# Performance work log

Measured on AMD Instinct MI355X. Metric: run time of the kernel, lower is better.

The kernel has to match this reference:

```python
import jax, jax.numpy as jnp
import numpy as np

N, P, G = 524288, 16, 8


def setup_inputs() -> dict:
    key = jax.random.key(0)
    k1, k2, k3, k4, k5 = jax.random.split(key, 5)
    # Strictly positive data (Box-Cox transform uses log / fractional powers)
    X = jax.random.uniform(k1, (N, P), dtype=jnp.float32) + 0.1
    # Box-Cox powers away from 0 to avoid division blow-up
    lambdas = jax.random.uniform(k2, (P, 1), dtype=jnp.float32) + 0.5
    # Means near the transformed-data range so densities don't underflow
    mus = 0.1 * jax.random.normal(k3, (G, P), dtype=jnp.float32) - 0.3
    # SPD covariances: 0.25*I + A A^T
    A = 0.05 * jax.random.normal(k4, (G, P, P), dtype=jnp.float32)
    sigmas = 0.25 * jnp.eye(P, dtype=jnp.float32)[None] + jnp.einsum('gpq,grq->gpr', A, A)
    w = jax.random.uniform(k5, (G, 1), dtype=jnp.float32)
    return {"X": X, "lambdas": lambdas, "mus": mus, "sigmas": sigmas, "w": w}


def reference(X, lambdas, mus, sigmas, w):
    # objective_fn of the GMM: negative log-likelihood of a Box-Cox GMM.
    n, p = X.shape
    lam = lambdas[:, 0]                                  # (p,)
    Xt = (X ** lam - 1.0) / lam                          # Box-Cox transform, (n,p)
    Sinv = jnp.linalg.inv(sigmas)                        # (G,p,p), once per component
    logdet = jnp.linalg.slogdet(sigmas)[1]               # (G,)
    d = Xt[:, None, :] - mus[None, :, :]                 # (n,G,p)
    quad = jnp.einsum('ngp,gpq,ngq->ng', d, Sinv, d)     # batched Mahalanobis, (n,G)
    lead = -0.5 * p * jnp.log(jnp.float32(2.0) * jnp.pi)
    jac = jnp.log(X) @ (lam - 1.0)                       # log-Jacobian of Box-Cox, (n,)
    ldens = -0.5 * quad + lead - 0.5 * logdet[None, :] + jac[:, None]  # (n,G)
    W = jax.nn.softmax(w[:, 0])                          # mixing proportions, (G,)
    mixed = (jnp.exp(ldens) * W).sum(-1)                 # (n,)
    return -jnp.log(mixed).sum()
```

## Files before the change

### kernel.cpp

```cpp
#include <hip/hip_runtime.h>
#include <hip/hip_bf16.h>


#define P 16
#define G 8

typedef short bf16x8 __attribute__((ext_vector_type(8)));
typedef unsigned u32x4v __attribute__((ext_vector_type(4)));
typedef float f32x16 __attribute__((ext_vector_type(16)));

__device__ __forceinline__ unsigned short f2bf(float f) {
    unsigned u = __builtin_bit_cast(unsigned, f);
    return (unsigned short)((u + 0x7FFFu + ((u >> 16) & 1u)) >> 16);
}

#define UFRAG_F 1024
#define WS_LC   1280
#define WS_LAM  1288
#define WS_LM1  1304
#define WS_RL   1320
#define WS_PART 4096

__global__ __launch_bounds__(128) void gmm_prep(const float* __restrict__ lambdas,
                                                const float* __restrict__ mus,
                                                const float* __restrict__ sigmas,
                                                const float* __restrict__ w,
                                                float* __restrict__ ws) {
    __shared__ float Ssh[G][P][P];
    __shared__ float Lsh[G][P][P];
    __shared__ float Vsh[G][P][P];
    __shared__ float u_sh[G][P];
    __shared__ float ldet[G];
    const int tid = threadIdx.x;
    const int g = tid >> 4;
    const int r = tid & 15;

    {
        const float4* src = (const float4*)(sigmas + g * P * P + r * P);
        float4* dst = (float4*)&Ssh[g][r][0];
        dst[0] = src[0]; dst[1] = src[1]; dst[2] = src[2]; dst[3] = src[3];
    }
    __syncthreads();

#pragma unroll
    for (int j = 0; j < P; ++j) {
        float s = Ssh[g][r][j];
#pragma unroll
        for (int k = 0; k < j; ++k) s -= Lsh[g][r][k] * Lsh[g][j][k];
        if (r == j) Lsh[g][j][j] = sqrtf(s);
        __syncthreads();
        if (r > j) Lsh[g][r][j] = s / Lsh[g][j][j];
        __syncthreads();
    }

    if (r == 0) {
        float ld = 0.f;
#pragma unroll
        for (int j = 0; j < P; ++j) ld += __logf(Lsh[g][j][j]);
        ldet[g] = 2.0f * ld;
    }

#pragma unroll
    for (int i = 0; i < P; ++i) {
        float s = 0.f;
#pragma unroll
        for (int k = 0; k < i; ++k) s += Lsh[g][i][k] * Vsh[g][k][r];
        const float rii = 1.0f / Lsh[g][i][i];
        Vsh[g][i][r] = (i == r) ? rii : ((i < r) ? 0.f : -s * rii);
    }
    __syncthreads();

    {
        float u = 0.f;
#pragma unroll
        for (int j = 0; j < P; ++j) u = fmaf(Vsh[g][r][j], mus[g * P + j], u);
        u_sh[g][r] = u;
    }
    __syncthreads();

    unsigned short* ws16 = (unsigned short*)ws;
    unsigned* wsu32 = (unsigned*)(ws + UFRAG_F);
#pragma unroll
    for (int pid = tid; pid < 256; pid += 128) {
        const int p = pid >> 6, ln = pid & 63;
        const int m = ln & 31, half = ln >> 5;
        const int grp = 2 * (pid >> 6) + (m >> 4), i = m & 15;
        unsigned short* dst = ws16 + (p * 64 + ln) * 8;
#pragma unroll
        for (int j = 0; j < 8; ++j) dst[j] = f2bf(Vsh[grp][i][half * 8 + j]);
        wsu32[p * 64 + ln] = (half == 0) ? (unsigned)f2bf(-u_sh[grp][i]) : 0u;
    }

    if (tid == 0) {
        float wm = w[0];
#pragma unroll
        for (int k = 1; k < G; ++k) wm = fmaxf(wm, w[k]);
        float s = 0.f;
#pragma unroll
        for (int k = 0; k < G; ++k) s += __expf(w[k] - wm);
        const float lse = wm + __logf(s);
        const float lead = -14.7030165f;
#pragma unroll
        for (int k = 0; k < G; ++k)
            ws[WS_LC + k] = (w[k] - lse) + lead - 0.5f * ldet[k];
    }
    if (tid < P) {
        float lam = lambdas[tid];
        ws[WS_LAM + tid] = lam;
        ws[WS_LM1 + tid] = lam - 1.0f;
        ws[WS_RL  + tid] = 1.0f / lam;
    }
}

__global__ __launch_bounds__(256, 4) void gmm_main(const float* __restrict__ X,
                                                   const float* __restrict__ ws,
                                                   float* __restrict__ partials,
                                                   int nrows) {
    __shared__ u32x4v sxt4[512];
    __shared__ float red[4];

    const int tid  = threadIdx.x;
    const int lane = tid & 63;
    const int wid  = tid >> 6;
    const unsigned short* ws16 = (const unsigned short*)ws;
    const unsigned* wsu32 = (const unsigned*)(ws + UFRAG_F);

    const bf16x8 av0 = *(const bf16x8*)(ws16 + (0 * 64 + lane) * 8);
    const bf16x8 av1 = *(const bf16x8*)(ws16 + (1 * 64 + lane) * 8);
    const bf16x8 av2 = *(const bf16x8*)(ws16 + (2 * 64 + lane) * 8);
    const bf16x8 av3 = *(const bf16x8*)(ws16 + (3 * 64 + lane) * 8);
    bf16x8 au0 = {0,0,0,0,0,0,0,0}; au0[0] = (short)wsu32[0 * 64 + lane];
    bf16x8 au1 = {0,0,0,0,0,0,0,0}; au1[0] = (short)wsu32[1 * 64 + lane];
    bf16x8 au2 = {0,0,0,0,0,0,0,0}; au2[0] = (short)wsu32[2 * 64 + lane];
    bf16x8 au3 = {0,0,0,0,0,0,0,0}; au3[0] = (short)wsu32[3 * 64 + lane];

    const int row = blockIdx.x * 256 + tid;
    const int rc = row < nrows ? row : nrows - 1;
    const float4* Xv = (const float4*)(X + (size_t)rc * P);
    const float4 A0 = Xv[0], A1 = Xv[1], A2 = Xv[2], A3 = Xv[3];

    float jac = 0.f;
#define XTP(i, xv_) \
    const float ln##i = __logf(xv_); \
    const float xt##i = (__expf(ws[WS_LAM + i] * ln##i) - 1.0f) * ws[WS_RL + i]; \
    jac = fmaf(ln##i, ws[WS_LM1 + i], jac);
    XTP(0, A0.x)  XTP(1, A0.y)  XTP(2, A0.z)  XTP(3, A0.w)
    XTP(4, A1.x)  XTP(5, A1.y)  XTP(6, A1.z)  XTP(7, A1.w)
    XTP(8, A2.x)  XTP(9, A2.y)  XTP(10, A2.z) XTP(11, A2.w)
    XTP(12, A3.x) XTP(13, A3.y) XTP(14, A3.z) XTP(15, A3.w)
#undef XTP

#define PK(h_, a_, b_) const unsigned w##h_ = (unsigned)f2bf(xt##a_) | ((unsigned)f2bf(xt##b_) << 16);
    PK(0, 0, 1)  PK(1, 2, 3)   PK(2, 4, 5)   PK(3, 6, 7)
    PK(4, 8, 9)  PK(5, 10, 11) PK(6, 12, 13) PK(7, 14, 15)
#undef PK
    {
        const u32x4v lo = {w0, w1, w2, w3};
        const u32x4v hi = {w4, w5, w6, w7};
        const int F = tid >> 5, c = tid & 31;
        sxt4[F * 64 + c]      = lo;
        sxt4[F * 64 + 32 + c] = hi;
    }
    __syncthreads();

    bf16x8 b1 = {0,0,0,0,0,0,0,0};
    if (lane < 32) b1[0] = (short)0x3F80;
    const bool h = (lane >= 32);

    float nll = 0.f;

#define PAIR(AV, AU, SA, SB) { \
    f32x16 acc = {}; \
    acc = __builtin_amdgcn_mfma_f32_32x32x16_bf16(AU, b1, acc, 0, 0, 0); \
    acc = __builtin_amdgcn_mfma_f32_32x32x16_bf16(AV, bx, acc, 0, 0, 0); \
    float sa = acc[0] * acc[0];    float sb = acc[8] * acc[8]; \
    sa = fmaf(acc[1], acc[1], sa); sb = fmaf(acc[9],  acc[9],  sb); \
    sa = fmaf(acc[2], acc[2], sa); sb = fmaf(acc[10], acc[10], sb); \
    sa = fmaf(acc[3], acc[3], sa); sb = fmaf(acc[11], acc[11], sb); \
    sa = fmaf(acc[4], acc[4], sa); sb = fmaf(acc[12], acc[12], sb); \
    sa = fmaf(acc[5], acc[5], sa); sb = fmaf(acc[13], acc[13], sb); \
    sa = fmaf(acc[6], acc[6], sa); sb = fmaf(acc[14], acc[14], sb); \
    sa = fmaf(acc[7], acc[7], sa); sb = fmaf(acc[15], acc[15], sb); \
    SA = sa; SB = sb; }

#define TILE(t_) { \
    const bf16x8 bx = __builtin_bit_cast(bf16x8, sxt4[(wid * 2 + t_) * 64 + lane]); \
    const float jn = __shfl(jac, t_ * 32 + (lane & 31), 64); \
    float pa0, pa1, pa2, pa3, pb0, pb1, pb2, pb3; \
    PAIR(av0, au0, pa0, pb0) PAIR(av1, au1, pa1, pb1) \
    PAIR(av2, au2, pa2, pb2) PAIR(av3, au3, pa3, pb3) \
    const float k0 = h ? pa2 : pa0, s0 = h ? pa0 : pa2; \
    const float k1 = h ? pb2 : pb0, s1 = h ? pb0 : pb2; \
    const float k2 = h ? pa3 : pa1, s2 = h ? pa1 : pa3; \
    const float k3 = h ? pb3 : pb1, s3 = h ? pb1 : pb3; \
    float m = 0.f; \
    { const float q = k0 + __shfl_xor(s0, 32, 64); m += __expf(fmaf(-0.5f, q, (h ? ws[WS_LC + 4] : ws[WS_LC + 0]) + jn)); } \
    { const float q = k1 + __shfl_xor(s1, 32, 64); m += __expf(fmaf(-0.5f, q, (h ? ws[WS_LC + 5] : ws[WS_LC + 1]) + jn)); } \
    { const float q = k2 + __shfl_xor(s2, 32, 64); m += __expf(fmaf(-0.5f, q, (h ? ws[WS_LC + 6] : ws[WS_LC + 2]) + jn)); } \
    { const float q = k3 + __shfl_xor(s3, 32, 64); m += __expf(fmaf(-0.5f, q, (h ? ws[WS_LC + 7] : ws[WS_LC + 3]) + jn)); } \
    m += __shfl_xor(m, 32, 64); \
    const int drow = blockIdx.x * 256 + wid * 64 + t_ * 32 + (lane & 31); \
    if (!h && drow < nrows) nll -= __logf(m); }

    TILE(0)
    TILE(1)
#undef TILE
#undef PAIR

#pragma unroll
    for (int off = 32; off > 0; off >>= 1) nll += __shfl_down(nll, off, 64);
    if (lane == 0) red[wid] = nll;
    __syncthreads();
    if (tid == 0) partials[blockIdx.x] = red[0] + red[1] + red[2] + red[3];
}

__global__ __launch_bounds__(256) void gmm_reduce(const float* __restrict__ partials,
                                                  float* __restrict__ out, int n) {
    __shared__ float red[4];
    const int tid = threadIdx.x;
    float s = 0.f;
    for (int i = tid; i < n; i += 256) s += partials[i];
#pragma unroll
    for (int off = 32; off > 0; off >>= 1) s += __shfl_down(s, off, 64);
    if ((tid & 63) == 0) red[tid >> 6] = s;
    __syncthreads();
    if (tid == 0) out[0] = red[0] + red[1] + red[2] + red[3];
}

extern "C" void kernel_launch(void* const* d_in, const int* in_sizes, int n_in,
                              void* d_out, int out_size, void* d_ws, size_t ws_size,
                              hipStream_t stream) {
    const float* X       = (const float*)d_in[0];
    const float* lambdas = (const float*)d_in[1];
    const float* mus     = (const float*)d_in[2];
    const float* sigmas  = (const float*)d_in[3];
    const float* w       = (const float*)d_in[4];
    float* out = (float*)d_out;
    float* ws  = (float*)d_ws;

    const int nrows = in_sizes[0] / P;
    const int nblocks = (nrows + 255) / 256;

    gmm_prep<<<1, 128, 0, stream>>>(lambdas, mus, sigmas, w, ws);
    gmm_main<<<nblocks, 256, 0, stream>>>(X, ws, ws + WS_PART, nrows);
    gmm_reduce<<<1, 256, 0, stream>>>(ws + WS_PART, out, nblocks);
}
```

Baseline: 97.56 us.

## Build MFMA B-fragments in registers and drop barriers in prep kernel

The main kernel no longer stages Box-Cox-transformed rows through shared memory. Each lane now loads half a row (8 floats) per tile, transforms it and packs it straight into its bf16 MFMA B fragment, combining the Jacobian halves with a cross-half shuffle. This removes the LDS round trip and a block-wide barrier. The prep kernel drops its __syncthreads and uses volatile shared arrays instead. That relies on each 16-thread component group running in lockstep inside one wavefront, which is an implicit-synchronisation risk.

```diff
diff --git a/kernel.cpp b/kernel.cpp
--- a/kernel.cpp
+++ b/kernel.cpp
@@ -6,7 +6,6 @@
 #define G 8
 
 typedef short bf16x8 __attribute__((ext_vector_type(8)));
-typedef unsigned u32x4v __attribute__((ext_vector_type(4)));
 typedef float f32x16 __attribute__((ext_vector_type(16)));
 
 __device__ __forceinline__ unsigned short f2bf(float f) {
@@ -26,38 +25,22 @@
                                                 const float* __restrict__ sigmas,
                                                 const float* __restrict__ w,
                                                 float* __restrict__ ws) {
-    __shared__ float Ssh[G][P][P];
-    __shared__ float Lsh[G][P][P];
-    __shared__ float Vsh[G][P][P];
-    __shared__ float u_sh[G][P];
-    __shared__ float ldet[G];
-    const int tid = threadIdx.x;
+    volatile __shared__ float Lsh[G][P][P];
+    volatile __shared__ float Vsh[G][P][P];
+    volatile __shared__ float ush[G][P];
+    const int tid  = threadIdx.x;
+    const int lane = tid & 63;
+    const int wid  = tid >> 6;
     const int g = tid >> 4;
     const int r = tid & 15;
 
-    {
-        const float4* src = (const float4*)(sigmas + g * P * P + r * P);
-        float4* dst = (float4*)&Ssh[g][r][0];
-        dst[0] = src[0]; dst[1] = src[1]; dst[2] = src[2]; dst[3] = src[3];
-    }
-    __syncthreads();
-
 #pragma unroll
     for (int j = 0; j < P; ++j) {
-        float s = Ssh[g][r][j];
+        float s = sigmas[g * P * P + r * P + j];
 #pragma unroll
         for (int k = 0; k < j; ++k) s -= Lsh[g][r][k] * Lsh[g][j][k];
         if (r == j) Lsh[g][j][j] = sqrtf(s);
-        __syncthreads();
-        if (r > j) Lsh[g][r][j] = s / Lsh[g][j][j];
-        __syncthreads();
-    }
-
-    if (r == 0) {
-        float ld = 0.f;
-#pragma unroll
-        for (int j = 0; j < P; ++j) ld += __logf(Lsh[g][j][j]);
-        ldet[g] = 2.0f * ld;
+        if (r > j)  Lsh[g][r][j] = s / Lsh[g][j][j];
     }
 
 #pragma unroll
@@ -68,42 +51,42 @@
         const float rii = 1.0f / Lsh[g][i][i];
         Vsh[g][i][r] = (i == r) ? rii : ((i < r) ? 0.f : -s * rii);
     }
-    __syncthreads();
 
     {
         float u = 0.f;
 #pragma unroll
         for (int j = 0; j < P; ++j) u = fmaf(Vsh[g][r][j], mus[g * P + j], u);
-        u_sh[g][r] = u;
-    }
-    __syncthreads();
+        ush[g][r] = u;
+    }
+
+    if (r == 0) {
+        float ld = 0.f;
+#pragma unroll
+        for (int j = 0; j < P; ++j) ld += __logf(Lsh[g][j][j]);
+        float wm = w[0];
+#pragma unroll
+        for (int k = 1; k < G; ++k) wm = fmaxf(wm, w[k]);
+        float ssum = 0.f;
+#pragma unroll
+        for (int k = 0; k < G; ++k) ssum += __expf(w[k] - wm);
+        const float lse = wm + __logf(ssum);
+        const float lead = -14.7030165f;
+        ws[WS_LC + g] = (w[g] - lse) + lead - ld;
+    }
 
     unsigned short* ws16 = (unsigned short*)ws;
     unsigned* wsu32 = (unsigned*)(ws + UFRAG_F);
 #pragma unroll
-    for (int pid = tid; pid < 256; pid += 128) {
-        const int p = pid >> 6, ln = pid & 63;
-        const int m = ln & 31, half = ln >> 5;
-        const int grp = 2 * (pid >> 6) + (m >> 4), i = m & 15;
-        unsigned short* dst = ws16 + (p * 64 + ln) * 8;
+    for (int pp = 0; pp < 2; ++pp) {
+        const int p = wid * 2 + pp;
+        const int m = lane & 31, half = lane >> 5;
+        const int grp = 2 * p + (m >> 4), i = m & 15;
+        unsigned short* dst = ws16 + (p * 64 + lane) * 8;
 #pragma unroll
         for (int j = 0; j < 8; ++j) dst[j] = f2bf(Vsh[grp][i][half * 8 + j]);
-        wsu32[p * 64 + ln] = (half == 0) ? (unsigned)f2bf(-u_sh[grp][i]) : 0u;
-    }
-
-    if (tid == 0) {
-        float wm = w[0];
-#pragma unroll
-        for (int k = 1; k < G; ++k) wm = fmaxf(wm, w[k]);
-        float s = 0.f;
-#pragma unroll
-        for (int k = 0; k < G; ++k) s += __expf(w[k] - wm);
-        const float lse = wm + __logf(s);
-        const float lead = -14.7030165f;
-#pragma unroll
-        for (int k = 0; k < G; ++k)
-            ws[WS_LC + k] = (w[k] - lse) + lead - 0.5f * ldet[k];
-    }
+        wsu32[p * 64 + lane] = (half == 0) ? (unsigned)f2bf(-ush[grp][i]) : 0u;
+    }
+
     if (tid < P) {
         float lam = lambdas[tid];
         ws[WS_LAM + tid] = lam;
@@ -116,12 +99,13 @@
                                                    const float* __restrict__ ws,
                                                    float* __restrict__ partials,
                                                    int nrows) {
-    __shared__ u32x4v sxt4[512];
     __shared__ float red[4];
 
     const int tid  = threadIdx.x;
     const int lane = tid & 63;
     const int wid  = tid >> 6;
+    const int n    = lane & 31;
+    const bool h   = (lane >= 32);
     const unsigned short* ws16 = (const unsigned short*)ws;
     const unsigned* wsu32 = (const unsigned*)(ws + UFRAG_F);
 
@@ -133,39 +117,17 @@
     bf16x8 au1 = {0,0,0,0,0,0,0,0}; au1[0] = (short)wsu32[1 * 64 + lane];
     bf16x8 au2 = {0,0,0,0,0,0,0,0}; au2[0] = (short)wsu32[2 * 64 + lane];
     bf16x8 au3 = {0,0,0,0,0,0,0,0}; au3[0] = (short)wsu32[3 * 64 + lane];
-
-    const int row = blockIdx.x * 256 + tid;
-    const int rc = row < nrows ? row : nrows - 1;
-    const float4* Xv = (const float4*)(X + (size_t)rc * P);
-    const float4 A0 = Xv[0], A1 = Xv[1], A2 = Xv[2], A3 = Xv[3];
-
-    float jac = 0.f;
-#define XTP(i, xv_) \
-    const float ln##i = __logf(xv_); \
-    const float xt##i = (__expf(ws[WS_LAM + i] * ln##i) - 1.0f) * ws[WS_RL + i]; \
-    jac = fmaf(ln##i, ws[WS_LM1 + i], jac);
-    XTP(0, A0.x)  XTP(1, A0.y)  XTP(2, A0.z)  XTP(3, A0.w)
-    XTP(4, A1.x)  XTP(5, A1.y)  XTP(6, A1.z)  XTP(7, A1.w)
-    XTP(8, A2.x)  XTP(9, A2.y)  XTP(10, A2.z) XTP(11, A2.w)
-    XTP(12, A3.x) XTP(13, A3.y) XTP(14, A3.z) XTP(15, A3.w)
-#undef XTP
-
-#define PK(h_, a_, b_) const unsigned w##h_ = (unsigned)f2bf(xt##a_) | ((unsigned)f2bf(xt##b_) << 16);
-    PK(0, 0, 1)  PK(1, 2, 3)   PK(2, 4, 5)   PK(3, 6, 7)
-    PK(4, 8, 9)  PK(5, 10, 11) PK(6, 12, 13) PK(7, 14, 15)
-#undef PK
-    {
-        const u32x4v lo = {w0, w1, w2, w3};
-        const u32x4v hi = {w4, w5, w6, w7};
-        const int F = tid >> 5, c = tid & 31;
-        sxt4[F * 64 + c]      = lo;
-        sxt4[F * 64 + 32 + c] = hi;
-    }
-    __syncthreads();
-
     bf16x8 b1 = {0,0,0,0,0,0,0,0};
-    if (lane < 32) b1[0] = (short)0x3F80;
-    const bool h = (lane >= 32);
+    if (!h) b1[0] = (short)0x3F80;
+
+#define SEL(base, e) (h ? ws[(base) + 8 + (e)] : ws[(base) + (e)])
+    const float la0 = SEL(WS_LAM,0), la1 = SEL(WS_LAM,1), la2 = SEL(WS_LAM,2), la3 = SEL(WS_LAM,3),
+                la4 = SEL(WS_LAM,4), la5 = SEL(WS_LAM,5), la6 = SEL(WS_LAM,6), la7 = SEL(WS_LAM,7);
+    const float lm0 = SEL(WS_LM1,0), lm1_ = SEL(WS_LM1,1), lm2 = SEL(WS_LM1,2), lm3 = SEL(WS_LM1,3),
+                lm4 = SEL(WS_LM1,4), lm5 = SEL(WS_LM1,5), lm6 = SEL(WS_LM1,6), lm7 = SEL(WS_LM1,7);
+    const float rl0 = SEL(WS_RL,0), rl1 = SEL(WS_RL,1), rl2 = SEL(WS_RL,2), rl3 = SEL(WS_RL,3),
+                rl4 = SEL(WS_RL,4), rl5 = SEL(WS_RL,5), rl6 = SEL(WS_RL,6), rl7 = SEL(WS_RL,7);
+#undef SEL
 
     float nll = 0.f;
 
@@ -184,8 +146,28 @@
     SA = sa; SB = sb; }
 
 #define TILE(t_) { \
-    const bf16x8 bx = __builtin_bit_cast(bf16x8, sxt4[(wid * 2 + t_) * 64 + lane]); \
-    const float jn = __shfl(jac, t_ * 32 + (lane & 31), 64); \
+    const int row = blockIdx.x * 256 + wid * 64 + t_ * 32 + n; \
+    const int rc = row < nrows ? row : nrows - 1; \
+    const float* xp = X + (size_t)rc * P + (h ? 8 : 0); \
+    const float4 xa = *(const float4*)xp; \
+    const float4 xb = *(const float4*)(xp + 4); \
+    float jp = 0.f; \
+    const float l0 = __logf(xa.x), l1 = __logf(xa.y), l2 = __logf(xa.z), l3 = __logf(xa.w); \
+    const float l4 = __logf(xb.x), l5 = __logf(xb.y), l6 = __logf(xb.z), l7 = __logf(xb.w); \
+    const float x0 = (__expf(la0 * l0) - 1.f) * rl0;  jp = fmaf(l0, lm0, jp); \
+    const float x1 = (__expf(la1 * l1) - 1.f) * rl1;  jp = fmaf(l1, lm1_, jp); \
+    const float x2 = (__expf(la2 * l2) - 1.f) * rl2;  jp = fmaf(l2, lm2, jp); \
+    const float x3 = (__expf(la3 * l3) - 1.f) * rl3;  jp = fmaf(l3, lm3, jp); \
+    const float x4 = (__expf(la4 * l4) - 1.f) * rl4;  jp = fmaf(l4, lm4, jp); \
+    const float x5 = (__expf(la5 * l5) - 1.f) * rl5;  jp = fmaf(l5, lm5, jp); \
+    const float x6 = (__expf(la6 * l6) - 1.f) * rl6;  jp = fmaf(l6, lm6, jp); \
+    const float x7 = (__expf(la7 * l7) - 1.f) * rl7;  jp = fmaf(l7, lm7, jp); \
+    bf16x8 bx; \
+    bx[0] = (short)f2bf(x0); bx[1] = (short)f2bf(x1); \
+    bx[2] = (short)f2bf(x2); bx[3] = (short)f2bf(x3); \
+    bx[4] = (short)f2bf(x4); bx[5] = (short)f2bf(x5); \
+    bx[6] = (short)f2bf(x6); bx[7] = (short)f2bf(x7); \
+    const float jn = jp + __shfl_xor(jp, 32, 64); \
     float pa0, pa1, pa2, pa3, pb0, pb1, pb2, pb3; \
     PAIR(av0, au0, pa0, pb0) PAIR(av1, au1, pa1, pb1) \
     PAIR(av2, au2, pa2, pb2) PAIR(av3, au3, pa3, pb3) \
@@ -199,8 +181,7 @@
     { const float q = k2 + __shfl_xor(s2, 32, 64); m += __expf(fmaf(-0.5f, q, (h ? ws[WS_LC + 6] : ws[WS_LC + 2]) + jn)); } \
     { const float q = k3 + __shfl_xor(s3, 32, 64); m += __expf(fmaf(-0.5f, q, (h ? ws[WS_LC + 7] : ws[WS_LC + 3]) + jn)); } \
     m += __shfl_xor(m, 32, 64); \
-    const int drow = blockIdx.x * 256 + wid * 64 + t_ * 32 + (lane & 31); \
-    if (!h && drow < nrows) nll -= __logf(m); }
+    if (!h && row < nrows) nll -= __logf(m); }
 
     TILE(0)
     TILE(1)
@@ -215,11 +196,11 @@
 }
 
 __global__ __launch_bounds__(256) void gmm_reduce(const float* __restrict__ partials,
-                                                  float* __restrict__ out, int n) {
+                                                  float* __restrict__ out, int nb) {
     __shared__ float red[4];
     const int tid = threadIdx.x;
     float s = 0.f;
-    for (int i = tid; i < n; i += 256) s += partials[i];
+    for (int i = tid; i < nb; i += 256) s += partials[i];
 #pragma unroll
     for (int off = 32; off > 0; off >>= 1) s += __shfl_down(s, off, 64);
     if ((tid & 63) == 0) red[tid >> 6] = s;
```

Measured after the change: 119.5 us. +22.5%, slower.

## Replace final reduce kernel with slotted atomic accumulation and hardware bf16 pack

Applied to the files above, without the earlier changes.

Drops the separate single-block reduction kernel. Each block now atomically adds its partial sum into one of 64 padded slots, and the last block to finish in each slot forwards that slot's total atomically into the output; the prep kernel zeroes the slots, counters and output. This removes one kernel launch and its serialized tail. It also swaps the manual bf16 rounding for the packed float2-to-bf16x2 intrinsic. In exchange it adds atomic contention, nondeterministic summation order, and the extra zeroing work in prep.

```diff
diff --git a/kernel.cpp b/kernel.cpp
--- a/kernel.cpp
+++ b/kernel.cpp
@@ -12,6 +12,12 @@
 __device__ __forceinline__ unsigned short f2bf(float f) {
     unsigned u = __builtin_bit_cast(unsigned, f);
     return (unsigned short)((u + 0x7FFFu + ((u >> 16) & 1u)) >> 16);
+}
+__device__ __forceinline__ unsigned pk2bf(float a, float b) {
+    __hip_bfloat162 h = __float22bfloat162_rn(make_float2(a, b));
+    unsigned u;
+    __builtin_memcpy(&u, &h, 4);
+    return u;
 }
 
 #define UFRAG_F 1024
@@ -19,13 +25,15 @@
 #define WS_LAM  1288
 #define WS_LM1  1304
 #define WS_RL   1320
-#define WS_PART 4096
+#define WS_SLOT 4096
+#define WS_CNT  6144
 
 __global__ __launch_bounds__(128) void gmm_prep(const float* __restrict__ lambdas,
                                                 const float* __restrict__ mus,
                                                 const float* __restrict__ sigmas,
                                                 const float* __restrict__ w,
-                                                float* __restrict__ ws) {
+                                                float* __restrict__ ws,
+                                                float* __restrict__ out) {
     __shared__ float Ssh[G][P][P];
     __shared__ float Lsh[G][P][P];
     __shared__ float Vsh[G][P][P];
@@ -35,6 +43,12 @@
     const int g = tid >> 4;
     const int r = tid & 15;
 
+    for (int i = tid; i < 2048; i += 128) {
+        ws[WS_SLOT + i] = 0.f;
+        ((unsigned*)(ws + WS_CNT))[i] = 0u;
+    }
+    if (tid == 0) out[0] = 0.f;
+
     {
         const float4* src = (const float4*)(sigmas + g * P * P + r * P);
         float4* dst = (float4*)&Ssh[g][r][0];
@@ -84,7 +98,7 @@
     for (int pid = tid; pid < 256; pid += 128) {
         const int p = pid >> 6, ln = pid & 63;
         const int m = ln & 31, half = ln >> 5;
-        const int grp = 2 * (pid >> 6) + (m >> 4), i = m & 15;
+        const int grp = 2 * p + (m >> 4), i = m & 15;
         unsigned short* dst = ws16 + (p * 64 + ln) * 8;
 #pragma unroll
         for (int j = 0; j < 8; ++j) dst[j] = f2bf(Vsh[grp][i][half * 8 + j]);
@@ -114,8 +128,9 @@
 
 __global__ __launch_bounds__(256, 4) void gmm_main(const float* __restrict__ X,
                                                    const float* __restrict__ ws,
-                                                   float* __restrict__ partials,
-                                                   int nrows) {
+                                                   float* __restrict__ wsrw,
+                                                   float* __restrict__ out,
+                                                   int nrows, int nblocks) {
     __shared__ u32x4v sxt4[512];
     __shared__ float red[4];
 
@@ -150,13 +165,11 @@
     XTP(12, A3.x) XTP(13, A3.y) XTP(14, A3.z) XTP(15, A3.w)
 #undef XTP
 
-#define PK(h_, a_, b_) const unsigned w##h_ = (unsigned)f2bf(xt##a_) | ((unsigned)f2bf(xt##b_) << 16);
-    PK(0, 0, 1)  PK(1, 2, 3)   PK(2, 4, 5)   PK(3, 6, 7)
-    PK(4, 8, 9)  PK(5, 10, 11) PK(6, 12, 13) PK(7, 14, 15)
-#undef PK
     {
-        const u32x4v lo = {w0, w1, w2, w3};
-        const u32x4v hi = {w4, w5, w6, w7};
+        const u32x4v lo = {pk2bf(xt0, xt1),   pk2bf(xt2, xt3),
+                           pk2bf(xt4, xt5),   pk2bf(xt6, xt7)};
+        const u32x4v hi = {pk2bf(xt8, xt9),   pk2bf(xt10, xt11),
+                           pk2bf(xt12, xt13), pk2bf(xt14, xt15)};
         const int F = tid >> 5, c = tid & 31;
         sxt4[F * 64 + c]      = lo;
         sxt4[F * 64 + 32 + c] = hi;
@@ -211,20 +224,20 @@
     for (int off = 32; off > 0; off >>= 1) nll += __shfl_down(nll, off, 64);
     if (lane == 0) red[wid] = nll;
     __syncthreads();
-    if (tid == 0) partials[blockIdx.x] = red[0] + red[1] + red[2] + red[3];
-}
-
-__global__ __launch_bounds__(256) void gmm_reduce(const float* __restrict__ partials,
-                                                  float* __restrict__ out, int n) {
-    __shared__ float red[4];
-    const int tid = threadIdx.x;
-    float s = 0.f;
-    for (int i = tid; i < n; i += 256) s += partials[i];
-#pragma unroll
-    for (int off = 32; off > 0; off >>= 1) s += __shfl_down(s, off, 64);
-    if ((tid & 63) == 0) red[tid >> 6] = s;
-    __syncthreads();
-    if (tid == 0) out[0] = red[0] + red[1] + red[2] + red[3];
+
+    if (tid == 0) {
+        const float bsum = red[0] + red[1] + red[2] + red[3];
+        const int s = blockIdx.x & 63;
+        float* slotp = wsrw + WS_SLOT + s * 32;
+        unsigned* cntp = (unsigned*)(wsrw + WS_CNT) + s * 32;
+        atomicAdd(slotp, bsum);
+        __threadfence();
+        const unsigned expected = (unsigned)((nblocks - s + 63) >> 6);
+        if (atomicAdd(cntp, 1u) + 1u == expected) {
+            const float ssum = atomicAdd(slotp, 0.0f);
+            atomicAdd(out, ssum);
+        }
+    }
 }
 
 extern "C" void kernel_launch(void* const* d_in, const int* in_sizes, int n_in,
@@ -241,7 +254,6 @@
     const int nrows = in_sizes[0] / P;
     const int nblocks = (nrows + 255) / 256;
 
-    gmm_prep<<<1, 128, 0, stream>>>(lambdas, mus, sigmas, w, ws);
-    gmm_main<<<nblocks, 256, 0, stream>>>(X, ws, ws + WS_PART, nrows);
-    gmm_reduce<<<1, 256, 0, stream>>>(ws + WS_PART, out, nblocks);
-}
+    gmm_prep<<<1, 128, 0, stream>>>(lambdas, mus, sigmas, w, ws, out);
+    gmm_main<<<nblocks, 256, 0, stream>>>(X, ws, ws, out, nrows, nblocks);
+}
```

New measurement: 126.8 us. +29.9%, slower.
